# Kernel optimization log

Measured on AMD Instinct MI355X. Metric: run time of the kernel, lower is better.

Reference implementation:

```python
import jax, jax.numpy as jnp
import numpy as np

BOX_WARP = 1.0
TRIPLANE_DEPTH = 1
PLANES = jnp.array([[[1, 0, 0], [0, 1, 0], [0, 0, 1]],
                    [[1, 0, 0], [0, 0, 1], [0, 1, 0]],
                    [[0, 1, 0], [0, 0, 1], [1, 0, 0]]], dtype=jnp.float32)
INV_PLANES = jnp.linalg.inv(PLANES)  # [3,3,3]


def project_onto_planes(coords):
    # coords [N,M,3] -> projections [N*3, M, 3] (bmm with inverse plane axes)
    N, M, _ = coords.shape
    proj = jnp.einsum('nmc,pcd->npmd', coords, INV_PLANES)
    return proj.reshape(N * 3, M, 3)


def grid_sample_3d(feat, grid):
    # torch.nn.functional.grid_sample 5D, mode=bilinear(trilinear), padding_mode=zeros,
    # align_corners=False. feat [B,C,D,H,W], grid [B,M,3] with (x->W, y->H, z->D).
    B, C, D, H, W = feat.shape
    x = ((grid[..., 0] + 1.0) * W - 1.0) * 0.5
    y = ((grid[..., 1] + 1.0) * H - 1.0) * 0.5
    z = ((grid[..., 2] + 1.0) * D - 1.0) * 0.5
    x0f = jnp.floor(x); y0f = jnp.floor(y); z0f = jnp.floor(z)
    wx = x - x0f; wy = y - y0f; wz = z - z0f
    x0 = x0f.astype(jnp.int32); y0 = y0f.astype(jnp.int32); z0 = z0f.astype(jnp.int32)
    feat_flat = feat.reshape(B, C, D * H * W)

    def corner(zi, yi, xi, w):
        valid = ((zi >= 0) & (zi < D) & (yi >= 0) & (yi < H) & (xi >= 0) & (xi < W))
        idx = (jnp.clip(zi, 0, D - 1) * H + jnp.clip(yi, 0, H - 1)) * W + jnp.clip(xi, 0, W - 1)
        v = jnp.take_along_axis(feat_flat, idx[:, None, :], axis=2)  # [B,C,M]
        return v * (w * valid)[:, None, :]

    out = (corner(z0, y0, x0, (1 - wz) * (1 - wy) * (1 - wx))
           + corner(z0, y0, x0 + 1, (1 - wz) * (1 - wy) * wx)
           + corner(z0, y0 + 1, x0, (1 - wz) * wy * (1 - wx))
           + corner(z0, y0 + 1, x0 + 1, (1 - wz) * wy * wx)
           + corner(z0 + 1, y0, x0, wz * (1 - wy) * (1 - wx))
           + corner(z0 + 1, y0, x0 + 1, wz * (1 - wy) * wx)
           + corner(z0 + 1, y0 + 1, x0, wz * wy * (1 - wx))
           + corner(z0 + 1, y0 + 1, x0 + 1, wz * wy * wx))
    return out  # [B,C,M]


def sample_from_planes(plane_feats_list, coordinates):
    N, M, _ = coordinates.shape
    proj = project_onto_planes(coordinates * (2.0 / BOX_WARP))  # [N*3,M,3]
    out = None
    for pf in plane_feats_list:
        _, P, CD, H, W = pf.shape
        C = CD // TRIPLANE_DEPTH
        f = pf.reshape(N * 3, C, TRIPLANE_DEPTH, H, W)
        s = grid_sample_3d(f, proj)  # [N*3,C,M]
        s = s.reshape(N, 3, C, M).transpose(0, 1, 3, 2)  # [N,3,M,C]
        out = s if out is None else out + s
    return out / len(plane_feats_list)


def ray_march(colors, densities, depths):
    # MipRayMarcher2 (EG3D): midpoint sampling, softplus(d-1) activation, alpha compositing.
    deltas = depths[:, :, 1:] - depths[:, :, :-1]                    # [N,R,S-1,1]
    cmid = 0.5 * (colors[:, :, :-1] + colors[:, :, 1:])
    dmid = 0.5 * (densities[:, :, :-1] + densities[:, :, 1:])
    dmid = jax.nn.softplus(dmid - 1.0)
    alpha = 1.0 - jnp.exp(-dmid * deltas)                            # [N,R,S-1,1]
    shifted = jnp.concatenate([jnp.ones_like(alpha[:, :, :1]), 1.0 - alpha + 1e-10], axis=2)
    weights = alpha * jnp.cumprod(shifted, axis=2)[:, :, :-1]
    rgb = jnp.sum(weights * cmid, axis=2)                            # [N,R,3]
    return rgb


def setup_inputs() -> dict:
    key = jax.random.key(0)
    ks = jax.random.split(key, 6)
    N, C = 4, 32
    R, S = 4096, 48
    M = R * S
    plane_lo = jax.random.normal(ks[0], (N, 3, C, 256, 256), jnp.float32) * 0.1
    plane_hi = jax.random.normal(ks[1], (N, 3, C, 512, 512), jnp.float32) * 0.1
    coordinates = jax.random.uniform(ks[2], (N, M, 3), jnp.float32, -0.45, 0.45)
    depths = 2.25 + 1.2 * jnp.sort(jax.random.uniform(ks[3], (N, R, S, 1), jnp.float32), axis=2)
    w_sigma = jax.random.normal(ks[4], (C, 1), jnp.float32) * 0.1
    w_rgb = jax.random.normal(ks[5], (C, 3), jnp.float32) * 0.1
    return {"plane_lo": plane_lo, "plane_hi": plane_hi, "coordinates": coordinates,
            "depths": depths, "w_sigma": w_sigma, "w_rgb": w_rgb}


def reference(plane_lo, plane_hi, coordinates, depths, w_sigma, w_rgb):
    N, R, S, _ = depths.shape
    feats = sample_from_planes([plane_lo, plane_hi], coordinates).mean(axis=1)  # [N,M,C]
    sigma = feats @ w_sigma                                                      # [N,M,1]
    rgb = jax.nn.sigmoid(feats @ w_rgb)                                          # [N,M,3]
    return ray_march(rgb.reshape(N, R, S, 3), sigma.reshape(N, R, S, 1), depths)
```

## Files before the change

### kernel.cpp

```cpp
#include <hip/hip_runtime.h>
#include <hip/hip_bf16.h>
#include <cstdint>

#define N_IMG 4
#define C_CH 32
#define R_RAYS 4096
#define S_SAMP 48
#define M_PTS (R_RAYS * S_SAMP)

__device__ __forceinline__ unsigned short f2bf(float f) {
  __hip_bfloat16 h = __float2bfloat16(f);
  return *reinterpret_cast<unsigned short*>(&h);
}

__global__ __launch_bounds__(256) void project_planes(
    const float* __restrict__ in, const float* __restrict__ w_sigma,
    const float* __restrict__ w_rgb, uint2* __restrict__ out, int logW) {
  __shared__ float sw[4 * C_CH];
  int t = threadIdx.x;
  if (t < C_CH) sw[t * 4] = w_sigma[t];
  if (t < 3 * C_CH) sw[(t / 3) * 4 + 1 + (t % 3)] = w_rgb[t];
  __syncthreads();

  int tid = blockIdx.x * 256 + t;
  int hw = tid & ((1 << (2 * logW)) - 1);
  int np = tid >> (2 * logW);
  const float* base = in + ((size_t)np << (5 + 2 * logW)) + hw;
  float a0 = 0.f, a1 = 0.f, a2 = 0.f, a3 = 0.f;
#pragma unroll
  for (int c = 0; c < C_CH; ++c) {
    float f = base[(size_t)c << (2 * logW)];
    a0 += f * sw[c * 4 + 0];
    a1 += f * sw[c * 4 + 1];
    a2 += f * sw[c * 4 + 2];
    a3 += f * sw[c * 4 + 3];
  }
  uint2 o;
  o.x = (unsigned)f2bf(a0) | ((unsigned)f2bf(a1) << 16);
  o.y = (unsigned)f2bf(a2) | ((unsigned)f2bf(a3) << 16);
  out[tid] = o;
}

__device__ __forceinline__ void upk(uint2 u, float* f) {
  f[0] = __uint_as_float(u.x << 16);
  f[1] = __uint_as_float(u.x & 0xffff0000u);
  f[2] = __uint_as_float(u.y << 16);
  f[3] = __uint_as_float(u.y & 0xffff0000u);
}

__global__ __launch_bounds__(256) void gather_pts(
    const float* __restrict__ coords,
    const uint2* __restrict__ lo_p,
    const uint2* __restrict__ hi_p,
    float4* __restrict__ pts)
{
  int idx = blockIdx.x * 256 + threadIdx.x;
  int n = idx / M_PTS;

  float X = coords[idx * 3 + 0] * 2.f;
  float Y = coords[idx * 3 + 1] * 2.f;
  float Z = coords[idx * 3 + 2] * 2.f;

  float acc0 = 0.f, acc1 = 0.f, acc2 = 0.f, acc3 = 0.f;
  const float gxs[3] = {X, X, Y};
  const float gys[3] = {Y, Z, Z};
  const float gzs[3] = {Z, Y, X};

#pragma unroll
  for (int p = 0; p < 3; ++p) {
    float wz = (1.f - 0.5f * fabsf(gzs[p])) * (1.f / 6.f);
#pragma unroll
    for (int lev = 0; lev < 2; ++lev) {
      const int logW = lev ? 9 : 8;
      const int W = 1 << logW;
      const uint2* pl = lev ? hi_p : lo_p;
      float xf = ((gxs[p] + 1.f) * (float)W - 1.f) * 0.5f;
      float yf = ((gys[p] + 1.f) * (float)W - 1.f) * 0.5f;
      float x0f = floorf(xf), y0f = floorf(yf);
      float fx = xf - x0f, fy = yf - y0f;
      int x0 = (int)x0f, y0 = (int)y0f;
      x0 = min(max(x0, 0), W - 2);
      y0 = min(max(y0, 0), W - 2);
      int base = ((((n * 3 + p) << logW) + y0) << logW) + x0;
      uint2 t00 = pl[base],     t01 = pl[base + 1];
      uint2 t10 = pl[base + W], t11 = pl[base + W + 1];
      float w00 = wz * (1.f - fy) * (1.f - fx);
      float w01 = wz * (1.f - fy) * fx;
      float w10 = wz * fy * (1.f - fx);
      float w11 = wz * fy * fx;
      float f00[4], f01[4], f10[4], f11[4];
      upk(t00, f00); upk(t01, f01); upk(t10, f10); upk(t11, f11);
      acc0 += w00 * f00[0] + w01 * f01[0] + w10 * f10[0] + w11 * f11[0];
      acc1 += w00 * f00[1] + w01 * f01[1] + w10 * f10[1] + w11 * f11[1];
      acc2 += w00 * f00[2] + w01 * f01[2] + w10 * f10[2] + w11 * f11[2];
      acc3 += w00 * f00[3] + w01 * f01[3] + w10 * f10[3] + w11 * f11[3];
    }
  }

  float4 o;
  o.x = 1.f / (1.f + __expf(-acc1));
  o.y = 1.f / (1.f + __expf(-acc2));
  o.z = 1.f / (1.f + __expf(-acc3));
  o.w = acc0;
  pts[idx] = o;
}

__global__ __launch_bounds__(256) void ray_march_k(
    const float4* __restrict__ pts, const float* __restrict__ depths,
    float* __restrict__ out) {
  int t = blockIdx.x * 256 + threadIdx.x;
  const float4* p = pts + (size_t)t * S_SAMP;
  const float* d = depths + (size_t)t * S_SAMP;

  float4 prev = p[0];
  float dprev = d[0];
  float T = 1.f, accR = 0.f, accG = 0.f, accB = 0.f;
#pragma unroll 4
  for (int i = 1; i < S_SAMP; ++i) {
    float4 cur = p[i];
    float dcur = d[i];
    float delta = dcur - dprev;
    float cr = 0.5f * (prev.x + cur.x);
    float cg = 0.5f * (prev.y + cur.y);
    float cb = 0.5f * (prev.z + cur.z);
    float dm = 0.5f * (prev.w + cur.w) - 1.f;
    float sp = fmaxf(dm, 0.f) + log1pf(__expf(-fabsf(dm)));
    float a = 1.f - __expf(-sp * delta);
    float w = a * T;
    accR += w * cr; accG += w * cg; accB += w * cb;
    T *= (1.f - a + 1e-10f);
    prev = cur; dprev = dcur;
  }
  out[t * 3 + 0] = accR;
  out[t * 3 + 1] = accG;
  out[t * 3 + 2] = accB;
}

extern "C" void kernel_launch(void* const* d_in, const int* in_sizes, int n_in,
                              void* d_out, int out_size, void* d_ws, size_t ws_size,
                              hipStream_t stream) {
  const float* plane_lo = (const float*)d_in[0];
  const float* plane_hi = (const float*)d_in[1];
  const float* coords   = (const float*)d_in[2];
  const float* depths   = (const float*)d_in[3];
  const float* w_sigma  = (const float*)d_in[4];
  const float* w_rgb    = (const float*)d_in[5];

  const size_t LO_TEX = (size_t)12 * 256 * 256;
  const size_t HI_TEX = (size_t)12 * 512 * 512;
  char* ws = (char*)d_ws;
  uint2* lo_p = (uint2*)ws;
  uint2* hi_p = (uint2*)(ws + LO_TEX * 8);
  float4* pts = (float4*)(ws + (LO_TEX + HI_TEX) * 8);

  project_planes<<<(int)(LO_TEX / 256), 256, 0, stream>>>(
      plane_lo, w_sigma, w_rgb, lo_p, 8);
  project_planes<<<(int)(HI_TEX / 256), 256, 0, stream>>>(
      plane_hi, w_sigma, w_rgb, hi_p, 9);

  gather_pts<<<(N_IMG * M_PTS) / 256, 256, 0, stream>>>(
      coords, lo_p, hi_p, pts);

  ray_march_k<<<(N_IMG * R_RAYS) / 256, 256, 0, stream>>>(
      pts, depths, (float*)d_out);
}
```

Before: 184.0 us.

## Fuse gather with ray march via shared memory and vectorize plane projection

Merges the per-point gather kernel and the ray-march kernel into one kernel. Each block samples the points of 16 rays into padded shared memory, then 16 threads march those rays, so the float4 intermediate buffer is never written to or read from global memory. The two plane-projection launches are merged into one launch, and each thread now handles four texels with vector loads and wide stores. Neighbouring bilinear taps are fetched with 16-byte loads. The trade-off is that only 16 of 256 threads do the serial march while the rest sit idle, and the 16-byte tap loads may be unaligned.

Result: slower. 201.0 us (+9.2%).

```diff
diff --git a/kernel.cpp b/kernel.cpp
--- a/kernel.cpp
+++ b/kernel.cpp
@@ -7,133 +7,157 @@
 #define R_RAYS 4096
 #define S_SAMP 48
 #define M_PTS (R_RAYS * S_SAMP)
+#define RAYS_PER_BLOCK 16
+#define PTS_PER_BLOCK (RAYS_PER_BLOCK * S_SAMP)
 
-__device__ __forceinline__ unsigned short f2bf(float f) {
+typedef float f32x4 __attribute__((ext_vector_type(4)));
+typedef unsigned int u32x4 __attribute__((ext_vector_type(4)));
+
+__device__ __forceinline__ unsigned f2bf(float f) {
   __hip_bfloat16 h = __float2bfloat16(f);
-  return *reinterpret_cast<unsigned short*>(&h);
+  return (unsigned)*reinterpret_cast<unsigned short*>(&h);
 }
+__device__ __forceinline__ float bflo(unsigned u) { return __uint_as_float(u << 16); }
+__device__ __forceinline__ float bfhi(unsigned u) { return __uint_as_float(u & 0xffff0000u); }
+
+#define LO_GROUPS 196608
+#define LO_BLOCKS 768
+#define HI_BLOCKS 3072
 
 __global__ __launch_bounds__(256) void project_planes(
-    const float* __restrict__ in, const float* __restrict__ w_sigma,
-    const float* __restrict__ w_rgb, uint2* __restrict__ out, int logW) {
+    const float* __restrict__ lo, const float* __restrict__ hi,
+    const float* __restrict__ w_sigma, const float* __restrict__ w_rgb,
+    uint4* __restrict__ lo_out, uint4* __restrict__ hi_out) {
   __shared__ float sw[4 * C_CH];
   int t = threadIdx.x;
   if (t < C_CH) sw[t * 4] = w_sigma[t];
   if (t < 3 * C_CH) sw[(t / 3) * 4 + 1 + (t % 3)] = w_rgb[t];
   __syncthreads();
 
-  int tid = blockIdx.x * 256 + t;
-  int hw = tid & ((1 << (2 * logW)) - 1);
-  int np = tid >> (2 * logW);
+  int bid = blockIdx.x;
+  const float* in;
+  uint4* out;
+  int logW, g;
+  if (bid < LO_BLOCKS) { in = lo; out = lo_out; logW = 8; g = bid * 256 + t; }
+  else { in = hi; out = hi_out; logW = 9; g = (bid - LO_BLOCKS) * 256 + t; }
+
+  int hw = (g * 4) & ((1 << (2 * logW)) - 1);
+  int np = (g * 4) >> (2 * logW);
   const float* base = in + ((size_t)np << (5 + 2 * logW)) + hw;
-  float a0 = 0.f, a1 = 0.f, a2 = 0.f, a3 = 0.f;
+
+  f32x4 as = 0.f, ar = 0.f, ag = 0.f, ab = 0.f;
 #pragma unroll
   for (int c = 0; c < C_CH; ++c) {
-    float f = base[(size_t)c << (2 * logW)];
-    a0 += f * sw[c * 4 + 0];
-    a1 += f * sw[c * 4 + 1];
-    a2 += f * sw[c * 4 + 2];
-    a3 += f * sw[c * 4 + 3];
+    f32x4 f;
+    __builtin_memcpy(&f, base + ((size_t)c << (2 * logW)), 16);
+    as += f * sw[c * 4 + 0];
+    ar += f * sw[c * 4 + 1];
+    ag += f * sw[c * 4 + 2];
+    ab += f * sw[c * 4 + 3];
   }
-  uint2 o;
-  o.x = (unsigned)f2bf(a0) | ((unsigned)f2bf(a1) << 16);
-  o.y = (unsigned)f2bf(a2) | ((unsigned)f2bf(a3) << 16);
-  out[tid] = o;
+  uint4 o0, o1;
+  o0.x = f2bf(as.x) | (f2bf(ar.x) << 16);
+  o0.y = f2bf(ag.x) | (f2bf(ab.x) << 16);
+  o0.z = f2bf(as.y) | (f2bf(ar.y) << 16);
+  o0.w = f2bf(ag.y) | (f2bf(ab.y) << 16);
+  o1.x = f2bf(as.z) | (f2bf(ar.z) << 16);
+  o1.y = f2bf(ag.z) | (f2bf(ab.z) << 16);
+  o1.z = f2bf(as.w) | (f2bf(ar.w) << 16);
+  o1.w = f2bf(ag.w) | (f2bf(ab.w) << 16);
+  out[g * 2 + 0] = o0;
+  out[g * 2 + 1] = o1;
 }
 
-__device__ __forceinline__ void upk(uint2 u, float* f) {
-  f[0] = __uint_as_float(u.x << 16);
-  f[1] = __uint_as_float(u.x & 0xffff0000u);
-  f[2] = __uint_as_float(u.y << 16);
-  f[3] = __uint_as_float(u.y & 0xffff0000u);
-}
-
-__global__ __launch_bounds__(256) void gather_pts(
+__global__ __launch_bounds__(256) void gather_march(
     const float* __restrict__ coords,
     const uint2* __restrict__ lo_p,
     const uint2* __restrict__ hi_p,
-    float4* __restrict__ pts)
-{
-  int idx = blockIdx.x * 256 + threadIdx.x;
-  int n = idx / M_PTS;
-
-  float X = coords[idx * 3 + 0] * 2.f;
-  float Y = coords[idx * 3 + 1] * 2.f;
-  float Z = coords[idx * 3 + 2] * 2.f;
-
-  float acc0 = 0.f, acc1 = 0.f, acc2 = 0.f, acc3 = 0.f;
-  const float gxs[3] = {X, X, Y};
-  const float gys[3] = {Y, Z, Z};
-  const float gzs[3] = {Z, Y, X};
+    const float* __restrict__ depths,
+    float* __restrict__ out) {
+  __shared__ float4 sp[PTS_PER_BLOCK + RAYS_PER_BLOCK];
+  __shared__ float  sd[PTS_PER_BLOCK + RAYS_PER_BLOCK];
+  int t = threadIdx.x;
+  int blockBase = blockIdx.x * PTS_PER_BLOCK;
+  int n = blockIdx.x >> 8;
 
 #pragma unroll
-  for (int p = 0; p < 3; ++p) {
-    float wz = (1.f - 0.5f * fabsf(gzs[p])) * (1.f / 6.f);
+  for (int k = 0; k < 3; ++k) {
+    int l = t + k * 256;
+    int gidx = blockBase + l;
+    float X = coords[gidx * 3 + 0] * 2.f;
+    float Y = coords[gidx * 3 + 1] * 2.f;
+    float Z = coords[gidx * 3 + 2] * 2.f;
+
+    float acc0 = 0.f, acc1 = 0.f, acc2 = 0.f, acc3 = 0.f;
+    const float gxs[3] = {X, X, Y};
+    const float gys[3] = {Y, Z, Z};
+    const float gzs[3] = {Z, Y, X};
+
 #pragma unroll
-    for (int lev = 0; lev < 2; ++lev) {
-      const int logW = lev ? 9 : 8;
-      const int W = 1 << logW;
-      const uint2* pl = lev ? hi_p : lo_p;
-      float xf = ((gxs[p] + 1.f) * (float)W - 1.f) * 0.5f;
-      float yf = ((gys[p] + 1.f) * (float)W - 1.f) * 0.5f;
-      float x0f = floorf(xf), y0f = floorf(yf);
-      float fx = xf - x0f, fy = yf - y0f;
-      int x0 = (int)x0f, y0 = (int)y0f;
-      x0 = min(max(x0, 0), W - 2);
-      y0 = min(max(y0, 0), W - 2);
-      int base = ((((n * 3 + p) << logW) + y0) << logW) + x0;
-      uint2 t00 = pl[base],     t01 = pl[base + 1];
-      uint2 t10 = pl[base + W], t11 = pl[base + W + 1];
-      float w00 = wz * (1.f - fy) * (1.f - fx);
-      float w01 = wz * (1.f - fy) * fx;
-      float w10 = wz * fy * (1.f - fx);
-      float w11 = wz * fy * fx;
-      float f00[4], f01[4], f10[4], f11[4];
-      upk(t00, f00); upk(t01, f01); upk(t10, f10); upk(t11, f11);
-      acc0 += w00 * f00[0] + w01 * f01[0] + w10 * f10[0] + w11 * f11[0];
-      acc1 += w00 * f00[1] + w01 * f01[1] + w10 * f10[1] + w11 * f11[1];
-      acc2 += w00 * f00[2] + w01 * f01[2] + w10 * f10[2] + w11 * f11[2];
-      acc3 += w00 * f00[3] + w01 * f01[3] + w10 * f10[3] + w11 * f11[3];
+    for (int p = 0; p < 3; ++p) {
+      float wz = (1.f - 0.5f * fabsf(gzs[p])) * (1.f / 6.f);
+#pragma unroll
+      for (int lev = 0; lev < 2; ++lev) {
+        const int logW = lev ? 9 : 8;
+        const int W = 1 << logW;
+        const uint2* pl = lev ? hi_p : lo_p;
+        float xf = ((gxs[p] + 1.f) * (float)W - 1.f) * 0.5f;
+        float yf = ((gys[p] + 1.f) * (float)W - 1.f) * 0.5f;
+        float x0f = floorf(xf), y0f = floorf(yf);
+        float fx = xf - x0f, fy = yf - y0f;
+        int x0 = (int)x0f, y0 = (int)y0f;
+        x0 = min(max(x0, 0), W - 2);
+        y0 = min(max(y0, 0), W - 2);
+        int base = ((((n * 3 + p) << logW) + y0) << logW) + x0;
+        u32x4 r0, r1;
+        __builtin_memcpy(&r0, pl + base, 16);
+        __builtin_memcpy(&r1, pl + base + W, 16);
+        float w00 = wz * (1.f - fy) * (1.f - fx);
+        float w01 = wz * (1.f - fy) * fx;
+        float w10 = wz * fy * (1.f - fx);
+        float w11 = wz * fy * fx;
+        acc0 += w00 * bflo(r0.x) + w01 * bflo(r0.z) + w10 * bflo(r1.x) + w11 * bflo(r1.z);
+        acc1 += w00 * bfhi(r0.x) + w01 * bfhi(r0.z) + w10 * bfhi(r1.x) + w11 * bfhi(r1.z);
+        acc2 += w00 * bflo(r0.y) + w01 * bflo(r0.w) + w10 * bflo(r1.y) + w11 * bflo(r1.w);
+        acc3 += w00 * bfhi(r0.y) + w01 * bfhi(r0.w) + w10 * bfhi(r1.y) + w11 * bfhi(r1.w);
+      }
     }
+    float4 o;
+    o.x = 1.f / (1.f + __expf(-acc1));
+    o.y = 1.f / (1.f + __expf(-acc2));
+    o.z = 1.f / (1.f + __expf(-acc3));
+    o.w = acc0;
+    int sl = l + l / S_SAMP;
+    sp[sl] = o;
+    sd[sl] = depths[gidx];
   }
+  __syncthreads();
 
-  float4 o;
-  o.x = 1.f / (1.f + __expf(-acc1));
-  o.y = 1.f / (1.f + __expf(-acc2));
-  o.z = 1.f / (1.f + __expf(-acc3));
-  o.w = acc0;
-  pts[idx] = o;
-}
-
-__global__ __launch_bounds__(256) void ray_march_k(
-    const float4* __restrict__ pts, const float* __restrict__ depths,
-    float* __restrict__ out) {
-  int t = blockIdx.x * 256 + threadIdx.x;
-  const float4* p = pts + (size_t)t * S_SAMP;
-  const float* d = depths + (size_t)t * S_SAMP;
-
-  float4 prev = p[0];
-  float dprev = d[0];
-  float T = 1.f, accR = 0.f, accG = 0.f, accB = 0.f;
-#pragma unroll 4
-  for (int i = 1; i < S_SAMP; ++i) {
-    float4 cur = p[i];
-    float dcur = d[i];
-    float delta = dcur - dprev;
-    float cr = 0.5f * (prev.x + cur.x);
-    float cg = 0.5f * (prev.y + cur.y);
-    float cb = 0.5f * (prev.z + cur.z);
-    float dm = 0.5f * (prev.w + cur.w) - 1.f;
-    float sp = fmaxf(dm, 0.f) + log1pf(__expf(-fabsf(dm)));
-    float a = 1.f - __expf(-sp * delta);
-    float w = a * T;
-    accR += w * cr; accG += w * cg; accB += w * cb;
-    T *= (1.f - a + 1e-10f);
-    prev = cur; dprev = dcur;
+  if (t < RAYS_PER_BLOCK) {
+    int base = t * (S_SAMP + 1);
+    float4 prev = sp[base];
+    float dprev = sd[base];
+    float T = 1.f, aR = 0.f, aG = 0.f, aB = 0.f;
+    for (int i = 1; i < S_SAMP; ++i) {
+      float4 cur = sp[base + i];
+      float dcur = sd[base + i];
+      float delta = dcur - dprev;
+      float cr = 0.5f * (prev.x + cur.x);
+      float cg = 0.5f * (prev.y + cur.y);
+      float cb = 0.5f * (prev.z + cur.z);
+      float dm = 0.5f * (prev.w + cur.w) - 1.f;
+      float sp_ = fmaxf(dm, 0.f) + log1pf(__expf(-fabsf(dm)));
+      float a = 1.f - __expf(-sp_ * delta);
+      float w = a * T;
+      aR += w * cr; aG += w * cg; aB += w * cb;
+      T *= (1.f - a + 1e-10f);
+      prev = cur; dprev = dcur;
+    }
+    int gr = blockIdx.x * RAYS_PER_BLOCK + t;
+    out[gr * 3 + 0] = aR;
+    out[gr * 3 + 1] = aG;
+    out[gr * 3 + 2] = aB;
   }
-  out[t * 3 + 0] = accR;
-  out[t * 3 + 1] = accG;
-  out[t * 3 + 2] = accB;
 }
 
 extern "C" void kernel_launch(void* const* d_in, const int* in_sizes, int n_in,
@@ -147,20 +171,13 @@
   const float* w_rgb    = (const float*)d_in[5];
 
   const size_t LO_TEX = (size_t)12 * 256 * 256;
-  const size_t HI_TEX = (size_t)12 * 512 * 512;
   char* ws = (char*)d_ws;
   uint2* lo_p = (uint2*)ws;
   uint2* hi_p = (uint2*)(ws + LO_TEX * 8);
-  float4* pts = (float4*)(ws + (LO_TEX + HI_TEX) * 8);
 
-  project_planes<<<(int)(LO_TEX / 256), 256, 0, stream>>>(
-      plane_lo, w_sigma, w_rgb, lo_p, 8);
-  project_planes<<<(int)(HI_TEX / 256), 256, 0, stream>>>(
-      plane_hi, w_sigma, w_rgb, hi_p, 9);
+  project_planes<<<LO_BLOCKS + HI_BLOCKS, 256, 0, stream>>>(
+      plane_lo, plane_hi, w_sigma, w_rgb, (uint4*)lo_p, (uint4*)hi_p);
 
-  gather_pts<<<(N_IMG * M_PTS) / 256, 256, 0, stream>>>(
-      coords, lo_p, hi_p, pts);
-
-  ray_march_k<<<(N_IMG * R_RAYS) / 256, 256, 0, stream>>>(
-      pts, depths, (float*)d_out);
+  gather_march<<<(N_IMG * M_PTS) / PTS_PER_BLOCK, 256, 0, stream>>>(
+      coords, lo_p, hi_p, depths, (float*)d_out);
 }
```
